# Performance work log

Measured on AMD Instinct MI355X. Metric: run time of the kernel, lower is better.

Reference implementation:

```python
import jax, jax.numpy as jnp
import numpy as np

B, S, D = 4, 2048, 1024
H = 16
HD = D // H  # head_dim = 64

def setup_inputs() -> dict:
    key = jax.random.key(0)
    kx, kq, ko = jax.random.split(key, 3)
    # xavier-uniform-like scale for weights
    lim_qkv = (6.0 / (D + 3 * D)) ** 0.5
    lim_o = (6.0 / (D + D)) ** 0.5
    return {
        "x": jax.random.normal(kx, (B, S, D), dtype=jnp.float32),
        "w_qkv": jax.random.uniform(kq, (3 * D, D), jnp.float32, -lim_qkv, lim_qkv),
        "b_qkv": jnp.zeros((3 * D,), jnp.float32),
        "w_o": jax.random.uniform(ko, (D, D), jnp.float32, -lim_o, lim_o),
        "b_o": jnp.zeros((D,), jnp.float32),
    }

def reference(x, w_qkv, b_qkv, w_o, b_o):
    b, s, _ = x.shape
    # QKV projection: torch Linear computes x @ W^T + b
    qkv = jnp.einsum("bsd,ed->bse", x, w_qkv) + b_qkv          # [B,S,3D]
    qkv = qkv.reshape(b, s, H, 3 * HD).transpose(0, 2, 1, 3)    # [B,H,S,3*hd]
    q, k, v = jnp.split(qkv, 3, axis=-1)                        # each [B,H,S,hd]
    scale = 1.0 / jnp.sqrt(jnp.asarray(HD, dtype=q.dtype))
    logits = jnp.einsum("bhqd,bhkd->bhqk", q, k) * scale        # [B,H,S,S]
    attn = jax.nn.softmax(logits, axis=-1)
    vals = jnp.einsum("bhqk,bhkd->bhqd", attn, v)               # [B,H,S,hd]
    vals = vals.transpose(0, 2, 1, 3).reshape(b, s, H * HD)     # [B,S,D]
    return jnp.einsum("bsd,ed->bse", vals, w_o) + b_o
```

## Files before the change

### kernel.cpp

```cpp
#include <hip/hip_runtime.h>
#include <hip/hip_bf16.h>


typedef __attribute__((ext_vector_type(4))) float f32x4;
typedef __attribute__((ext_vector_type(8))) short s16x8;
typedef __attribute__((ext_vector_type(2))) unsigned u32x2;
typedef __attribute__((ext_vector_type(4))) unsigned u32x4;

constexpr size_t PART_ELEMS = (size_t)8192 * 1024;

__device__ __forceinline__ unsigned short f2bf(float f) {
  __hip_bfloat16 h = __float2bfloat16(f);
  unsigned short u;
  __builtin_memcpy(&u, &h, 2);
  return u;
}
__device__ __forceinline__ unsigned pack2bf(float a, float b) {
  return (unsigned)f2bf(a) | ((unsigned)f2bf(b) << 16);
}
__device__ __forceinline__ float bf2f(unsigned short u) {
  union { unsigned u; float f; } v; v.u = ((unsigned)u) << 16;
  return v.f;
}
__device__ __forceinline__ float fexp2(float x) {
#if __has_builtin(__builtin_amdgcn_exp2f)
  return __builtin_amdgcn_exp2f(x);
#else
  float r; asm("v_exp_f32 %0, %1" : "=v"(r) : "v"(x)); return r;
#endif
}
__device__ __forceinline__ void gload_lds16(const void* g, void* l) {
  __builtin_amdgcn_global_load_lds(
      (const __attribute__((address_space(1))) unsigned*)g,
      (__attribute__((address_space(3))) unsigned*)l, 16, 0, 0);
}
__device__ __forceinline__ int swzs(int row, int col) {
  return row * 64 + (((col >> 3) ^ (row & 7)) << 3) + (col & 7);
}

__global__ __launch_bounds__(256) void cvt_kernel(const float* __restrict__ in,
                                                  unsigned short* __restrict__ out) {
  const size_t i = ((size_t)blockIdx.x * 256 + threadIdx.x) * 8;
  f32x4 v0 = *reinterpret_cast<const f32x4*>(in + i);
  f32x4 v1 = *reinterpret_cast<const f32x4*>(in + i + 4);
  u32x4 pk;
  pk.x = pack2bf(v0.x, v0.y); pk.y = pack2bf(v0.z, v0.w);
  pk.z = pack2bf(v1.x, v1.y); pk.w = pack2bf(v1.z, v1.w);
  *reinterpret_cast<u32x4*>(out + i) = pk;
}

template <bool SCATTER>
__global__ __launch_bounds__(256) void gemm_bb(
    const unsigned short* __restrict__ A, const unsigned short* __restrict__ Bw,
    const float* __restrict__ bias, void* __restrict__ Cptr,
    int M, int N, int K) {
  __shared__ short lds_a[128 * 32];
  __shared__ short lds_b[128 * 32];
  const int t = threadIdx.x;
  const int l = t & 63;
  const int w = t >> 6;
  const int bm = blockIdx.y * 128;
  const int bn = blockIdx.x * 128;
  const int wr = (w >> 1) * 64;
  const int wc = (w & 1) * 64;
  const int lr = l & 15;
  const int lk = (l >> 4) * 8;

  f32x4 acc[4][4] = {};

  const int srow = w * 16 + (l >> 2);
  const int scol = (l & 3) * 8;
  short* adst0 = &lds_a[(w * 16) * 32];
  short* adst1 = &lds_a[(64 + w * 16) * 32];
  short* bdst0 = &lds_b[(w * 16) * 32];
  short* bdst1 = &lds_b[(64 + w * 16) * 32];

  for (int k0 = 0; k0 < K; k0 += 32) {
    const unsigned short* as = &A[(size_t)(bm + srow) * K + k0 + scol];
    gload_lds16(as, adst0);
    gload_lds16(as + (size_t)64 * K, adst1);
    const unsigned short* bs = &Bw[(size_t)(bn + srow) * K + k0 + scol];
    gload_lds16(bs, bdst0);
    gload_lds16(bs + (size_t)64 * K, bdst1);
    __syncthreads();

    s16x8 af[4], bfr[4];
#pragma unroll
    for (int mt = 0; mt < 4; ++mt)
      af[mt] = *reinterpret_cast<const s16x8*>(&lds_a[(wr + mt * 16 + lr) * 32 + lk]);
#pragma unroll
    for (int nt = 0; nt < 4; ++nt)
      bfr[nt] = *reinterpret_cast<const s16x8*>(&lds_b[(wc + nt * 16 + lr) * 32 + lk]);
#pragma unroll
    for (int mt = 0; mt < 4; ++mt)
#pragma unroll
      for (int nt = 0; nt < 4; ++nt)
        acc[mt][nt] = __builtin_amdgcn_mfma_f32_16x16x32_bf16(af[mt], bfr[nt], acc[mt][nt], 0, 0, 0);
    __syncthreads();
  }

#pragma unroll
  for (int mt = 0; mt < 4; ++mt) {
#pragma unroll
    for (int nt = 0; nt < 4; ++nt) {
#pragma unroll
      for (int r = 0; r < 4; ++r) {
        const int row = bm + wr + mt * 16 + (l >> 4) * 4 + r;
        const int col = bn + wc + nt * 16 + lr;
        const float vv = acc[mt][nt][r] + bias[col];
        if (SCATTER) {
          const int h = col / 192;
          const int rem = col - h * 192;
          const int part = rem >> 6;
          const int d = rem & 63;
          const int s = row & 2047;
          const size_t bh = (size_t)(row >> 11) * 16 + h;
          unsigned short* W = (unsigned short*)Cptr;
          float vvv = vv;
          if (part == 0) vvv *= 0.1803368801f;
          size_t off;
          if (part == 2)
            off = 2 * PART_ELEMS + (bh * 64 + d) * 2048 + s;
          else
            off = (size_t)part * PART_ELEMS + (bh * 2048 + s) * 64 + d;
          W[off] = f2bf(vvv);
        } else {
          ((float*)Cptr)[(size_t)row * N + col] = vv;
        }
      }
    }
  }
}

__global__ __launch_bounds__(512, 4) void attn_kernel(
    const unsigned short* __restrict__ ws, unsigned short* __restrict__ vals) {
  __shared__ short k_lds[64 * 64];
  __shared__ short vt_lds[64 * 64];
  __shared__ short p_lds[256 * 64];
  const int t = threadIdx.x;
  const int l = t & 63;
  const int w = t >> 6;
  const int lr = l & 15;
  const int lkh = l >> 4;
  const int f = blockIdx.x;
  const int xcd = f & 7;
  const int j = f >> 3;
  const int bh = xcd * 8 + (j & 7);
  const int qt = j >> 3;
  const int b = bh >> 4;
  const int h = bh & 15;
  const unsigned short* Qh  = ws + (size_t)bh * (2048 * 64);
  const unsigned short* Kh  = ws + PART_ELEMS + (size_t)bh * (2048 * 64);
  const unsigned short* VTh = ws + 2 * PART_ELEMS + (size_t)bh * (64 * 2048);

  const int srow = t >> 3;
  const int scol = (t & 7) * 8;

  s16x8 qf[2][2];
  {
    const unsigned short* qb = Qh + ((size_t)qt * 256 + w * 32 + lr) * 64 + lkh * 8;
    qf[0][0] = *reinterpret_cast<const s16x8*>(qb);
    qf[0][1] = *reinterpret_cast<const s16x8*>(qb + 32);
    qf[1][0] = *reinterpret_cast<const s16x8*>(qb + 16 * 64);
    qf[1][1] = *reinterpret_cast<const s16x8*>(qb + 16 * 64 + 32);
  }
  {
    s16x8 k0 = *reinterpret_cast<const s16x8*>(Kh + (size_t)srow * 64 + scol);
    s16x8 v0 = *reinterpret_cast<const s16x8*>(VTh + (size_t)srow * 2048 + scol);
    *reinterpret_cast<s16x8*>(&k_lds[swzs(srow, scol)])  = k0;
    *reinterpret_cast<s16x8*>(&vt_lds[swzs(srow, scol)]) = v0;
  }
  __syncthreads();

  f32x4 o_acc[2][4] = {};
  float m_s[2] = {-1e30f, -1e30f};
  float l_s[2] = {0.f, 0.f};

  for (int kt = 0; kt < 32; ++kt) {
    const bool pre = (kt + 1) < 32;

    s16x8 kr, vr;
    if (pre) {
      kr = *reinterpret_cast<const s16x8*>(Kh + ((size_t)(kt + 1) * 64 + srow) * 64 + scol);
      vr = *reinterpret_cast<const s16x8*>(VTh + (size_t)srow * 2048 + (kt + 1) * 64 + scol);
    }

    f32x4 s_acc[2][4] = {};
    {
      s16x8 kf[4][2];
#pragma unroll
      for (int nt = 0; nt < 4; ++nt) {
        kf[nt][0] = *reinterpret_cast<const s16x8*>(&k_lds[swzs(nt * 16 + lr, lkh * 8)]);
        kf[nt][1] = *reinterpret_cast<const s16x8*>(&k_lds[swzs(nt * 16 + lr, 32 + lkh * 8)]);
      }
#pragma unroll
      for (int qh = 0; qh < 2; ++qh)
#pragma unroll
        for (int nt = 0; nt < 4; ++nt) {
          s_acc[qh][nt] = __builtin_amdgcn_mfma_f32_16x16x32_bf16(kf[nt][0], qf[qh][0], s_acc[qh][nt], 0, 0, 0);
          s_acc[qh][nt] = __builtin_amdgcn_mfma_f32_16x16x32_bf16(kf[nt][1], qf[qh][1], s_acc[qh][nt], 0, 0, 0);
        }
    }

#pragma unroll
    for (int qh = 0; qh < 2; ++qh) {
      float mx = fmaxf(
          fmaxf(fmaxf(fmaxf(s_acc[qh][0][0], s_acc[qh][0][1]), fmaxf(s_acc[qh][0][2], s_acc[qh][0][3])),
                fmaxf(fmaxf(s_acc[qh][1][0], s_acc[qh][1][1]), fmaxf(s_acc[qh][1][2], s_acc[qh][1][3]))),
          fmaxf(fmaxf(fmaxf(s_acc[qh][2][0], s_acc[qh][2][1]), fmaxf(s_acc[qh][2][2], s_acc[qh][2][3])),
                fmaxf(fmaxf(s_acc[qh][3][0], s_acc[qh][3][1]), fmaxf(s_acc[qh][3][2], s_acc[qh][3][3]))));
      mx = fmaxf(mx, __shfl_xor(mx, 16));
      mx = fmaxf(mx, __shfl_xor(mx, 32));

      if (__any(mx > m_s[qh] + 8.0f)) {
        const float mnew = fmaxf(m_s[qh], mx);
        const float sc = fexp2(m_s[qh] - mnew);
        m_s[qh] = mnew;
        l_s[qh] *= sc;
#pragma unroll
        for (int r = 0; r < 4; ++r) {
          const float scr = __shfl(sc, 4 * lkh + r);
          o_acc[qh][0][r] *= scr; o_acc[qh][1][r] *= scr;
          o_acc[qh][2][r] *= scr; o_acc[qh][3][r] *= scr;
        }
      }

      float rs = 0.f;
#pragma unroll
      for (int nt = 0; nt < 4; ++nt) {
        float p0 = fexp2(s_acc[qh][nt][0] - m_s[qh]);
        float p1 = fexp2(s_acc[qh][nt][1] - m_s[qh]);
        float p2 = fexp2(s_acc[qh][nt][2] - m_s[qh]);
        float p3 = fexp2(s_acc[qh][nt][3] - m_s[qh]);
        rs += (p0 + p1) + (p2 + p3);
        u32x2 pk;
        pk.x = pack2bf(p0, p1);
        pk.y = pack2bf(p2, p3);
        *reinterpret_cast<u32x2*>(&p_lds[swzs(w * 32 + qh * 16 + lr, nt * 16 + 4 * lkh)]) = pk;
      }
      rs += __shfl_xor(rs, 16);
      rs += __shfl_xor(rs, 32);
      l_s[qh] += rs;
    }

    {
      s16x8 vf[4][2];
#pragma unroll
      for (int nt = 0; nt < 4; ++nt) {
        vf[nt][0] = *reinterpret_cast<const s16x8*>(&vt_lds[swzs(nt * 16 + lr, lkh * 8)]);
        vf[nt][1] = *reinterpret_cast<const s16x8*>(&vt_lds[swzs(nt * 16 + lr, 32 + lkh * 8)]);
      }
#pragma unroll
      for (int qh = 0; qh < 2; ++qh) {
        s16x8 pf0 = *reinterpret_cast<const s16x8*>(&p_lds[swzs(w * 32 + qh * 16 + lr, lkh * 8)]);
        s16x8 pf1 = *reinterpret_cast<const s16x8*>(&p_lds[swzs(w * 32 + qh * 16 + lr, 32 + lkh * 8)]);
#pragma unroll
        for (int nt = 0; nt < 4; ++nt) {
          o_acc[qh][nt] = __builtin_amdgcn_mfma_f32_16x16x32_bf16(pf0, vf[nt][0], o_acc[qh][nt], 0, 0, 0);
          o_acc[qh][nt] = __builtin_amdgcn_mfma_f32_16x16x32_bf16(pf1, vf[nt][1], o_acc[qh][nt], 0, 0, 0);
        }
      }
    }
    __syncthreads();

    if (pre) {
      *reinterpret_cast<s16x8*>(&k_lds[swzs(srow, scol)])  = kr;
      *reinterpret_cast<s16x8*>(&vt_lds[swzs(srow, scol)]) = vr;
    }
    __syncthreads();
  }

#pragma unroll
  for (int qh = 0; qh < 2; ++qh) {
#pragma unroll
    for (int r = 0; r < 4; ++r) {
      const float lv = __shfl(l_s[qh], 4 * lkh + r);
      const float inv = 1.0f / lv;
      const size_t row = (size_t)b * 2048 + qt * 256 + w * 32 + qh * 16 + lkh * 4 + r;
#pragma unroll
      for (int nt = 0; nt < 4; ++nt) {
        vals[row * 1024 + h * 64 + nt * 16 + lr] = f2bf(o_acc[qh][nt][r] * inv);
      }
    }
  }
}

extern "C" void kernel_launch(void* const* d_in, const int* in_sizes, int n_in,
                              void* d_out, int out_size, void* d_ws, size_t ws_size,
                              hipStream_t stream) {
  const float* x     = (const float*)d_in[0];
  const float* w_qkv = (const float*)d_in[1];
  const float* b_qkv = (const float*)d_in[2];
  const float* w_o   = (const float*)d_in[3];
  const float* b_o   = (const float*)d_in[4];
  float* out = (float*)d_out;

  unsigned short* xb     = (unsigned short*)d_ws;
  unsigned short* planes = xb + PART_ELEMS;
  unsigned short* wqkv_b = (unsigned short*)d_out;
  unsigned short* wo_b   = planes;

  cvt_kernel<<<4096, 256, 0, stream>>>(x, xb);
  cvt_kernel<<<1536, 256, 0, stream>>>(w_qkv, wqkv_b);
  gemm_bb<true><<<dim3(24, 64), 256, 0, stream>>>(
      xb, wqkv_b, b_qkv, planes, 8192, 3072, 1024);
  attn_kernel<<<512, 512, 0, stream>>>(planes, xb);
  cvt_kernel<<<512, 256, 0, stream>>>(w_o, wo_b);
  gemm_bb<false><<<dim3(8, 64), 256, 0, stream>>>(
      xb, wo_b, b_o, out, 8192, 1024, 1024);
}
```

Baseline: 231.2 us.

## Double-buffer attention K/V tiles, remap GEMM blocks per XCD, defer row-sum reduction

The attention kernel now double-buffers the K and V^T tiles in LDS, which removes one __syncthreads per key tile. It raises wave priority around the MFMA blocks and computes the row max with three-input max. The row-sum cross-lane shuffle moves out of the loop and runs once at the end, which is valid because the rescale factor is uniform across lanes of a row. The GEMMs switch to a 1D grid with an XCD-aware block mapping so each XCD works on adjacent M tiles for better L2 reuse. The extra LDS for the double buffer may lower occupancy.

```diff
diff --git a/kernel.cpp b/kernel.cpp
--- a/kernel.cpp
+++ b/kernel.cpp
@@ -28,6 +28,9 @@
 #else
   float r; asm("v_exp_f32 %0, %1" : "=v"(r) : "v"(x)); return r;
 #endif
+}
+__device__ __forceinline__ float max3f(float a, float b, float c) {
+  return fmaxf(fmaxf(a, b), c);
 }
 __device__ __forceinline__ void gload_lds16(const void* g, void* l) {
   __builtin_amdgcn_global_load_lds(
@@ -59,8 +62,11 @@
   const int t = threadIdx.x;
   const int l = t & 63;
   const int w = t >> 6;
-  const int bm = blockIdx.y * 128;
-  const int bn = blockIdx.x * 128;
+  const int id = blockIdx.x;
+  const int xcd = id & 7;
+  const int rr = id >> 3;
+  const int bm = (xcd * 8 + (rr & 7)) * 128;
+  const int bn = (rr >> 3) * 128;
   const int wr = (w >> 1) * 64;
   const int wc = (w & 1) * 64;
   const int lr = l & 15;
@@ -134,8 +140,8 @@
 
 __global__ __launch_bounds__(512, 4) void attn_kernel(
     const unsigned short* __restrict__ ws, unsigned short* __restrict__ vals) {
-  __shared__ short k_lds[64 * 64];
-  __shared__ short vt_lds[64 * 64];
+  __shared__ short k_lds[2][64 * 64];
+  __shared__ short vt_lds[2][64 * 64];
   __shared__ short p_lds[256 * 64];
   const int t = threadIdx.x;
   const int l = t & 63;
@@ -167,8 +173,8 @@
   {
     s16x8 k0 = *reinterpret_cast<const s16x8*>(Kh + (size_t)srow * 64 + scol);
     s16x8 v0 = *reinterpret_cast<const s16x8*>(VTh + (size_t)srow * 2048 + scol);
-    *reinterpret_cast<s16x8*>(&k_lds[swzs(srow, scol)])  = k0;
-    *reinterpret_cast<s16x8*>(&vt_lds[swzs(srow, scol)]) = v0;
+    *reinterpret_cast<s16x8*>(&k_lds[0][swzs(srow, scol)])  = k0;
+    *reinterpret_cast<s16x8*>(&vt_lds[0][swzs(srow, scol)]) = v0;
   }
   __syncthreads();
 
@@ -177,6 +183,8 @@
   float l_s[2] = {0.f, 0.f};
 
   for (int kt = 0; kt < 32; ++kt) {
+    const int cur = kt & 1;
+    const int nxt = cur ^ 1;
     const bool pre = (kt + 1) < 32;
 
     s16x8 kr, vr;
@@ -190,9 +198,10 @@
       s16x8 kf[4][2];
 #pragma unroll
       for (int nt = 0; nt < 4; ++nt) {
-        kf[nt][0] = *reinterpret_cast<const s16x8*>(&k_lds[swzs(nt * 16 + lr, lkh * 8)]);
-        kf[nt][1] = *reinterpret_cast<const s16x8*>(&k_lds[swzs(nt * 16 + lr, 32 + lkh * 8)]);
-      }
+        kf[nt][0] = *reinterpret_cast<const s16x8*>(&k_lds[cur][swzs(nt * 16 + lr, lkh * 8)]);
+        kf[nt][1] = *reinterpret_cast<const s16x8*>(&k_lds[cur][swzs(nt * 16 + lr, 32 + lkh * 8)]);
+      }
+      __builtin_amdgcn_s_setprio(1);
 #pragma unroll
       for (int qh = 0; qh < 2; ++qh)
 #pragma unroll
@@ -200,15 +209,18 @@
           s_acc[qh][nt] = __builtin_amdgcn_mfma_f32_16x16x32_bf16(kf[nt][0], qf[qh][0], s_acc[qh][nt], 0, 0, 0);
           s_acc[qh][nt] = __builtin_amdgcn_mfma_f32_16x16x32_bf16(kf[nt][1], qf[qh][1], s_acc[qh][nt], 0, 0, 0);
         }
+      __builtin_amdgcn_s_setprio(0);
     }
 
 #pragma unroll
     for (int qh = 0; qh < 2; ++qh) {
-      float mx = fmaxf(
-          fmaxf(fmaxf(fmaxf(s_acc[qh][0][0], s_acc[qh][0][1]), fmaxf(s_acc[qh][0][2], s_acc[qh][0][3])),
-                fmaxf(fmaxf(s_acc[qh][1][0], s_acc[qh][1][1]), fmaxf(s_acc[qh][1][2], s_acc[qh][1][3]))),
-          fmaxf(fmaxf(fmaxf(s_acc[qh][2][0], s_acc[qh][2][1]), fmaxf(s_acc[qh][2][2], s_acc[qh][2][3])),
-                fmaxf(fmaxf(s_acc[qh][3][0], s_acc[qh][3][1]), fmaxf(s_acc[qh][3][2], s_acc[qh][3][3]))));
+      float mx = max3f(max3f(s_acc[qh][0][0], s_acc[qh][0][1], s_acc[qh][0][2]),
+                       max3f(s_acc[qh][0][3], s_acc[qh][1][0], s_acc[qh][1][1]),
+                       max3f(s_acc[qh][1][2], s_acc[qh][1][3], s_acc[qh][2][0]));
+      mx = max3f(mx,
+                 max3f(s_acc[qh][2][1], s_acc[qh][2][2], s_acc[qh][2][3]),
+                 max3f(s_acc[qh][3][0], s_acc[qh][3][1], s_acc[qh][3][2]));
+      mx = fmaxf(mx, s_acc[qh][3][3]);
       mx = fmaxf(mx, __shfl_xor(mx, 16));
       mx = fmaxf(mx, __shfl_xor(mx, 32));
 
@@ -238,8 +250,6 @@
         pk.y = pack2bf(p2, p3);
         *reinterpret_cast<u32x2*>(&p_lds[swzs(w * 32 + qh * 16 + lr, nt * 16 + 4 * lkh)]) = pk;
       }
-      rs += __shfl_xor(rs, 16);
-      rs += __shfl_xor(rs, 32);
       l_s[qh] += rs;
     }
 
@@ -247,9 +257,10 @@
       s16x8 vf[4][2];
 #pragma unroll
       for (int nt = 0; nt < 4; ++nt) {
-        vf[nt][0] = *reinterpret_cast<const s16x8*>(&vt_lds[swzs(nt * 16 + lr, lkh * 8)]);
-        vf[nt][1] = *reinterpret_cast<const s16x8*>(&vt_lds[swzs(nt * 16 + lr, 32 + lkh * 8)]);
-      }
+        vf[nt][0] = *reinterpret_cast<const s16x8*>(&vt_lds[cur][swzs(nt * 16 + lr, lkh * 8)]);
+        vf[nt][1] = *reinterpret_cast<const s16x8*>(&vt_lds[cur][swzs(nt * 16 + lr, 32 + lkh * 8)]);
+      }
+      __builtin_amdgcn_s_setprio(1);
 #pragma unroll
       for (int qh = 0; qh < 2; ++qh) {
         s16x8 pf0 = *reinterpret_cast<const s16x8*>(&p_lds[swzs(w * 32 + qh * 16 + lr, lkh * 8)]);
@@ -260,16 +271,21 @@
           o_acc[qh][nt] = __builtin_amdgcn_mfma_f32_16x16x32_bf16(pf1, vf[nt][1], o_acc[qh][nt], 0, 0, 0);
         }
       }
+      __builtin_amdgcn_s_setprio(0);
+    }
+
+    if (pre) {
+      *reinterpret_cast<s16x8*>(&k_lds[nxt][swzs(srow, scol)])  = kr;
+      *reinterpret_cast<s16x8*>(&vt_lds[nxt][swzs(srow, scol)]) = vr;
     }
     __syncthreads();
-
-    if (pre) {
-      *reinterpret_cast<s16x8*>(&k_lds[swzs(srow, scol)])  = kr;
-      *reinterpret_cast<s16x8*>(&vt_lds[swzs(srow, scol)]) = vr;
-    }
-    __syncthreads();
-  }
-
+  }
+
+#pragma unroll
+  for (int qh = 0; qh < 2; ++qh) {
+    l_s[qh] += __shfl_xor(l_s[qh], 16);
+    l_s[qh] += __shfl_xor(l_s[qh], 32);
+  }
 #pragma unroll
   for (int qh = 0; qh < 2; ++qh) {
 #pragma unroll
@@ -302,10 +318,10 @@
 
   cvt_kernel<<<4096, 256, 0, stream>>>(x, xb);
   cvt_kernel<<<1536, 256, 0, stream>>>(w_qkv, wqkv_b);
-  gemm_bb<true><<<dim3(24, 64), 256, 0, stream>>>(
+  gemm_bb<true><<<1536, 256, 0, stream>>>(
       xb, wqkv_b, b_qkv, planes, 8192, 3072, 1024);
   attn_kernel<<<512, 512, 0, stream>>>(planes, xb);
   cvt_kernel<<<512, 256, 0, stream>>>(w_o, wo_b);
-  gemm_bb<false><<<dim3(8, 64), 256, 0, stream>>>(
+  gemm_bb<false><<<512, 256, 0, stream>>>(
       xb, wo_b, b_o, out, 8192, 1024, 1024);
 }
```

Result: faster. 225.1 us (-2.7%).
